# Kernel tuning notes

Hardware: AMD Instinct MI355X
Metric: run time of the kernel (lower is better)

The kernel has to match this reference:

```python
import jax, jax.numpy as jnp
import numpy as np

N = 100000      # nodes
E = 1600000     # edges (avg degree 16)
F_IN = 128      # num_features
H = 64          # hidden_dim
C = 7           # num_classes


def setup_inputs() -> dict:
    key = jax.random.key(0)
    ks = jax.random.split(key, 9)
    x = jax.random.normal(ks[0], (N, F_IN), dtype=jnp.float32)
    edge_index = jax.random.randint(ks[1], (2, E), 0, N, dtype=jnp.int32)
    s1 = 1.0 / np.sqrt(F_IN)
    s2 = 1.0 / np.sqrt(H)
    # SAGEConv1: lin_l applied to aggregated neighbors, lin_r to root
    W1l = jax.random.uniform(ks[2], (F_IN, H), jnp.float32, -s1, s1)
    W1r = jax.random.uniform(ks[3], (F_IN, H), jnp.float32, -s1, s1)
    b1 = jax.random.uniform(ks[4], (H,), jnp.float32, -s1, s1)
    # SAGEConv2
    W2l = jax.random.uniform(ks[5], (H, C), jnp.float32, -s2, s2)
    W2r = jax.random.uniform(ks[6], (H, C), jnp.float32, -s2, s2)
    b2 = jax.random.uniform(ks[7], (C,), jnp.float32, -s2, s2)
    return {"x": x, "edge_index": edge_index, "W1l": W1l, "W1r": W1r,
            "b1": b1, "W2l": W2l, "W2r": W2r, "b2": b2}


def _segment_mean(vals, idx, num_segments):
    # scatter-mean: sum messages per destination node, divide by in-degree
    sums = jax.ops.segment_sum(vals, idx, num_segments=num_segments)
    cnt = jax.ops.segment_sum(jnp.ones(idx.shape, vals.dtype), idx,
                              num_segments=num_segments)
    return sums / jnp.maximum(cnt, 1.0)[:, None]


def reference(x, edge_index, W1l, W1r, b1, W2l, W2r, b2):
    src, dst = edge_index[0], edge_index[1]
    # SAGEConv 1: mean of neighbor (src) features at each dst, plus root term
    agg1 = _segment_mean(x[src], dst, N)              # [N, F_IN]
    h = agg1 @ W1l + x @ W1r + b1                     # [N, H]
    h = jax.nn.relu(h)
    # dropout is inactive in eval mode (deterministic reference)
    # SAGEConv 2
    agg2 = _segment_mean(h[src], dst, N)              # [N, H]
    out = agg2 @ W2l + h @ W2r + b2                   # [N, C]
    return jax.nn.log_softmax(out, axis=1)
```

## Files before the change

### kernel.cpp

```cpp
#include <hip/hip_runtime.h>
#include <cstdint>
#include <cstddef>


#define CAP 64
#define BINSZ 128
#define CH 16384

typedef __attribute__((ext_vector_type(8))) short bf16x8v;
typedef __attribute__((ext_vector_type(4))) float f32x4v;

__device__ __forceinline__ float bf2f(unsigned short u) {
  return __uint_as_float(((unsigned int)u) << 16);
}
__device__ __forceinline__ unsigned short f2bf(float f) {
  unsigned int x = __float_as_uint(f);
  unsigned int r = (x + 0x7fffu + ((x >> 16) & 1u)) >> 16;
  return (unsigned short)r;
}

__global__ __launch_bounds__(256) void k_hist(const int* __restrict__ ei,
                                              int* __restrict__ hist,
                                              int E, int NB, int NCH) {
  __shared__ int lcnt[1024];
  const int c = blockIdx.x, t = threadIdx.x;
  for (int i = t; i < NB; i += 256) lcnt[i] = 0;
  __syncthreads();
  const int base = c * CH;
  const int end = min(base + CH, E);
  for (int e = base + t; e < end; e += 256) {
    int d = ei[E + e];
    atomicAdd(&lcnt[d >> 7], 1);
  }
  __syncthreads();
  for (int i = t; i < NB; i += 256) hist[(size_t)i * NCH + c] = lcnt[i];
}

__global__ __launch_bounds__(256) void k_scanA(int* __restrict__ hist,
                                               int* __restrict__ tot,
                                               int NB, int NCH) {
  const int lane = threadIdx.x & 63;
  const int bin = blockIdx.x * 4 + (threadIdx.x >> 6);
  if (bin >= NB) return;
  int* h = hist + (size_t)bin * NCH;
  int carry = 0;
  for (int base = 0; base < NCH; base += 64) {
    int i = base + lane;
    int v = (i < NCH) ? h[i] : 0;
    int incl = v;
    #pragma unroll
    for (int d = 1; d < 64; d <<= 1) {
      int t = __shfl_up(incl, d, 64);
      if (lane >= d) incl += t;
    }
    if (i < NCH) h[i] = carry + incl - v;
    carry += __shfl(incl, 63, 64);
  }
  if (lane == 0) tot[bin] = carry;
}

__global__ __launch_bounds__(64) void k_scanB(const int* __restrict__ tot,
                                              int* __restrict__ binbase, int NB) {
  const int lane = threadIdx.x;
  int carry = 0;
  for (int base = 0; base < NB; base += 64) {
    int i = base + lane;
    int v = (i < NB) ? tot[i] : 0;
    int incl = v;
    #pragma unroll
    for (int d = 1; d < 64; d <<= 1) {
      int t = __shfl_up(incl, d, 64);
      if (lane >= d) incl += t;
    }
    if (i < NB) binbase[i] = carry + incl - v;
    carry += __shfl(incl, 63, 64);
  }
  if (lane == 0) binbase[NB] = carry;
}

__global__ __launch_bounds__(256) void k_scat(const int* __restrict__ ei,
                                              const int* __restrict__ hist,
                                              const int* __restrict__ binbase,
                                              unsigned int* __restrict__ part,
                                              int E, int NB, int NCH) {
  __shared__ int lcur[1024];
  const int c = blockIdx.x, t = threadIdx.x;
  for (int i = t; i < NB; i += 256)
    lcur[i] = hist[(size_t)i * NCH + c] + binbase[i];
  __syncthreads();
  const int base = c * CH;
  const int end = min(base + CH, E);
  for (int e = base + t; e < end; e += 256) {
    int s = ei[e];
    int d = ei[E + e];
    int bin = d >> 7;
    int pos = atomicAdd(&lcur[bin], 1);
    part[pos] = (unsigned)s | ((unsigned)(d & 127) << 17);
  }
}

__global__ __launch_bounds__(256) void k_bucketB(const int* __restrict__ binbase,
                                                 const unsigned int* __restrict__ part,
                                                 int* __restrict__ cnt,
                                                 int* __restrict__ bucket) {
  __shared__ int lbkt[BINSZ * CAP];
  __shared__ int ldeg[BINSZ];
  const int b = blockIdx.x, t = threadIdx.x;
  if (t < BINSZ) ldeg[t] = 0;
  __syncthreads();
  const int e0 = binbase[b], e1 = binbase[b + 1];
  for (int i = e0 + t; i < e1; i += 256) {
    unsigned rec = part[i];
    int loc = rec >> 17;
    int p = atomicAdd(&ldeg[loc], 1);
    if (p < CAP) lbkt[loc * CAP + p] = (int)(rec & 0x1FFFFu);
  }
  __syncthreads();
  if (t < BINSZ) cnt[b * BINSZ + t] = ldeg[t];
  const int4* s4 = (const int4*)lbkt;
  int4* d4 = (int4*)(bucket + (size_t)b * BINSZ * CAP);
  #pragma unroll 2
  for (int i = t; i < BINSZ * CAP / 4; i += 256) d4[i] = s4[i];
}

__global__ __launch_bounds__(256) void k_wprep(const float* __restrict__ W1l,
                                               const float* __restrict__ W1r,
                                               unsigned short* __restrict__ wswz) {
  int idx = blockIdx.x * 256 + threadIdx.x;
  int j = idx & 7;
  int lane = (idx >> 3) & 63;
  int c = (idx >> 9) & 7;
  int t4 = idx >> 12;
  int kk = t4 * 32 + (lane >> 4) * 8 + j;
  int nn = c * 16 + (lane & 15);
  float v = (nn < 64) ? W1l[kk * 64 + nn] : W1r[kk * 64 + (nn - 64)];
  wswz[idx] = f2bf(v);
}

__global__ __launch_bounds__(256) void k_gemm1(
    const float* __restrict__ x,
    const unsigned short* __restrict__ wswz,
    const float* __restrict__ b1,
    unsigned short* __restrict__ xl,
    unsigned short* __restrict__ hroot,
    int Nn) {
  __shared__ unsigned short Bsw[16384];
  const int t = threadIdx.x;
  {
    const uint4* src = (const uint4*)wswz;
    uint4* dst = (uint4*)Bsw;
    #pragma unroll
    for (int i = 0; i < 8; ++i) dst[t + i * 256] = src[t + i * 256];
  }
  __syncthreads();

  const int lane = t & 63;
  const int wid = t >> 6;
  const int quad = lane >> 4;
  const int m = lane & 15;
  const int rowA = blockIdx.x * 64 + wid * 16 + m;
  const float* xrow = x + (size_t)min(rowA, Nn - 1) * 128;

  f32x4v acc[8];
  #pragma unroll
  for (int c = 0; c < 8; ++c) acc[c] = (f32x4v){0.f, 0.f, 0.f, 0.f};

  #pragma unroll
  for (int t4 = 0; t4 < 4; ++t4) {
    const int koff = t4 * 32 + quad * 8;
    float4 a0 = *(const float4*)(xrow + koff);
    float4 a1 = *(const float4*)(xrow + koff + 4);
    bf16x8v af;
    af[0] = (short)f2bf(a0.x); af[1] = (short)f2bf(a0.y);
    af[2] = (short)f2bf(a0.z); af[3] = (short)f2bf(a0.w);
    af[4] = (short)f2bf(a1.x); af[5] = (short)f2bf(a1.y);
    af[6] = (short)f2bf(a1.z); af[7] = (short)f2bf(a1.w);
    #pragma unroll
    for (int c = 0; c < 8; ++c) {
      const bf16x8v bf_ = *(const bf16x8v*)&Bsw[(((t4 * 8 + c) * 64 + lane)) << 3];
      acc[c] = __builtin_amdgcn_mfma_f32_16x16x32_bf16(af, bf_, acc[c], 0, 0, 0);
    }
  }

  const int rbase = blockIdx.x * 64 + wid * 16 + quad * 4;
  #pragma unroll
  for (int c = 0; c < 8; ++c) {
    const int col = c * 16 + m;
    #pragma unroll
    for (int i = 0; i < 4; ++i) {
      const int r = rbase + i;
      if (r < Nn) {
        if (c < 4) xl[(size_t)r * 64 + col] = f2bf(acc[c][i]);
        else       hroot[(size_t)r * 64 + (col - 64)] = f2bf(acc[c][i] + b1[col - 64]);
      }
    }
  }
}

__global__ __launch_bounds__(256) void k_agg1(
    const int* __restrict__ cnt, const int* __restrict__ bucket,
    const unsigned short* __restrict__ xl, const unsigned short* __restrict__ hroot,
    unsigned short* __restrict__ hbuf, int Nn) {
  const int lane = threadIdx.x & 63;
  const int gw = blockIdx.x * (blockDim.x >> 6) + (threadIdx.x >> 6);
  const int nw = gridDim.x * (blockDim.x >> 6);
  for (int n = gw; n < Nn; n += nw) {
    int c = cnt[n];
    int m = c < CAP ? c : CAP;
    int sidx = (lane < m) ? bucket[(size_t)n * CAP + lane] : 0;
    if ((unsigned)sidx >= (unsigned)Nn) sidx = 0;
    float acc = 0.f;
    int i = 0;
    for (; i + 4 <= m; i += 4) {
      int s0 = __shfl(sidx, i, 64);
      int s1 = __shfl(sidx, i + 1, 64);
      int s2 = __shfl(sidx, i + 2, 64);
      int s3 = __shfl(sidx, i + 3, 64);
      float v0 = bf2f(xl[(size_t)s0 * 64 + lane]);
      float v1 = bf2f(xl[(size_t)s1 * 64 + lane]);
      float v2 = bf2f(xl[(size_t)s2 * 64 + lane]);
      float v3 = bf2f(xl[(size_t)s3 * 64 + lane]);
      acc += (v0 + v1) + (v2 + v3);
    }
    for (; i < m; ++i) {
      int s = __shfl(sidx, i, 64);
      acc += bf2f(xl[(size_t)s * 64 + lane]);
    }
    float dd = c > 0 ? (float)c : 1.f;
    float hv = acc / dd + bf2f(hroot[(size_t)n * 64 + lane]);
    hbuf[(size_t)n * 64 + lane] = f2bf(fmaxf(hv, 0.f));
  }
}

__global__ __launch_bounds__(128) void k_gemm2(
    const unsigned short* __restrict__ hbuf,
    const float* __restrict__ W2l, const float* __restrict__ W2r,
    const float* __restrict__ b2,
    float* __restrict__ hl, float* __restrict__ hr, int Nn) {
  __shared__ float tile[128 * 65];
  const int t = threadIdx.x;
  const int rowbase = blockIdx.x * 128;
  for (int idx = t; idx < 128 * 64; idx += 128) {
    int r = idx >> 6, k = idx & 63;
    int n = rowbase + r;
    tile[r * 65 + k] = (n < Nn) ? bf2f(hbuf[(size_t)n * 64 + k]) : 0.f;
  }
  __syncthreads();
  int n = rowbase + t;
  if (n >= Nn) return;
  float al[7] = {0, 0, 0, 0, 0, 0, 0};
  float ar[7] = {0, 0, 0, 0, 0, 0, 0};
  for (int k = 0; k < 64; ++k) {
    float hv = tile[t * 65 + k];
    #pragma unroll
    for (int c = 0; c < 7; ++c) {
      al[c] = fmaf(hv, W2l[k * 7 + c], al[c]);
      ar[c] = fmaf(hv, W2r[k * 7 + c], ar[c]);
    }
  }
  #pragma unroll
  for (int c = 0; c < 7; ++c) {
    hl[(size_t)n * 7 + c] = al[c];
    hr[(size_t)n * 7 + c] = ar[c] + b2[c];
  }
}

__global__ __launch_bounds__(256) void k_out(
    const int* __restrict__ cnt, const int* __restrict__ bucket,
    const float* __restrict__ hl, const float* __restrict__ hr,
    float* __restrict__ out, int Nn) {
  const int lane = threadIdx.x & 63;
  const int c = lane & 7;
  const int sub = lane >> 3;
  const int gw = blockIdx.x * (blockDim.x >> 6) + (threadIdx.x >> 6);
  const int n = gw * 8 + sub;
  if (n >= Nn) return;
  int cn = cnt[n];
  int m = cn < CAP ? cn : CAP;
  const bool act = (c < 7);
  float acc = 0.f;
  for (int e = 0; e < m; ++e) {
    int s = bucket[(size_t)n * CAP + e];
    if ((unsigned)s >= (unsigned)Nn) s = 0;
    if (act) acc += hl[(size_t)s * 7 + c];
  }
  float dd = cn > 0 ? (float)cn : 1.f;
  float v = act ? (acc / dd + hr[(size_t)n * 7 + c]) : -INFINITY;
  float mx = v;
  mx = fmaxf(mx, __shfl_xor(mx, 1, 8));
  mx = fmaxf(mx, __shfl_xor(mx, 2, 8));
  mx = fmaxf(mx, __shfl_xor(mx, 4, 8));
  float ex = act ? expf(v - mx) : 0.f;
  float s2 = ex;
  s2 += __shfl_xor(s2, 1, 8);
  s2 += __shfl_xor(s2, 2, 8);
  s2 += __shfl_xor(s2, 4, 8);
  float res = v - mx - logf(s2);
  if (act) out[(size_t)n * 7 + c] = res;
}

static inline size_t alignup(size_t v) { return (v + 255) & ~(size_t)255; }

extern "C" void kernel_launch(void* const* d_in, const int* in_sizes, int n_in,
                              void* d_out, int out_size, void* d_ws, size_t ws_size,
                              hipStream_t stream) {
  const int N = in_sizes[0] / 128;
  const int E = in_sizes[1] / 2;
  const int NB = (N + BINSZ - 1) / BINSZ;
  const int Np = NB * BINSZ;
  const int NCH = (E + CH - 1) / CH;

  const float* x   = (const float*)d_in[0];
  const int*   ei  = (const int*)d_in[1];
  const float* W1l = (const float*)d_in[2];
  const float* W1r = (const float*)d_in[3];
  const float* b1  = (const float*)d_in[4];
  const float* W2l = (const float*)d_in[5];
  const float* W2r = (const float*)d_in[6];
  const float* b2  = (const float*)d_in[7];
  float* out = (float*)d_out;

  char* p = (char*)d_ws;
  int* hist    = (int*)p;            p += alignup((size_t)NB * NCH * 4);
  int* tot     = (int*)p;            p += alignup((size_t)NB * 4);
  int* binbase = (int*)p;            p += alignup((size_t)(NB + 1) * 4);
  unsigned int* part = (unsigned int*)p; p += alignup((size_t)E * 4);
  int* cnt    = (int*)p;             p += alignup((size_t)Np * 4);
  int* bucket = (int*)p;             p += alignup((size_t)Np * CAP * 4);
  unsigned short* wswz = (unsigned short*)p; p += alignup((size_t)16384 * 2);
  unsigned short* xl    = (unsigned short*)p; p += alignup((size_t)N * 64 * 2);
  unsigned short* hroot = (unsigned short*)p; p += alignup((size_t)N * 64 * 2);
  unsigned short* hbuf  = (unsigned short*)p; p += alignup((size_t)N * 64 * 2);
  float* hl  = (float*)p;            p += alignup((size_t)N * 7 * 4);
  float* hr  = (float*)p;            p += alignup((size_t)N * 7 * 4);

  dim3 b256(256);
  k_hist<<<dim3(NCH), b256, 0, stream>>>(ei, hist, E, NB, NCH);
  k_scanA<<<dim3((NB + 3) / 4), b256, 0, stream>>>(hist, tot, NB, NCH);
  k_scanB<<<dim3(1), dim3(64), 0, stream>>>(tot, binbase, NB);
  k_scat<<<dim3(NCH), b256, 0, stream>>>(ei, hist, binbase, part, E, NB, NCH);
  k_bucketB<<<dim3(NB), b256, 0, stream>>>(binbase, part, cnt, bucket);
  k_wprep<<<dim3(64), b256, 0, stream>>>(W1l, W1r, wswz);
  k_gemm1<<<dim3((N + 63) / 64), b256, 0, stream>>>(x, wswz, b1, xl, hroot, N);
  k_agg1<<<dim3(2048), b256, 0, stream>>>(cnt, bucket, xl, hroot, hbuf, N);
  k_gemm2<<<dim3((N + 127) / 128), dim3(128), 0, stream>>>(hbuf, W2l, W2r, b2, hl, hr, N);
  const int waves_out = (N + 7) / 8;
  k_out<<<dim3((waves_out + 3) / 4), b256, 0, stream>>>(cnt, bucket, hl, hr, out, N);
}
```

Baseline: 282.6 us.

## Aggregate directly from binned edge records with shared-memory atomics, drop bucket CSR

Removes the per-node bucket-building kernel and its capped 64-neighbor bucket array. Both aggregation stages now read the destination-binned edge records and accumulate into per-bin shared-memory float accumulators with LDS atomics. This avoids writing and re-reading a large padded bucket array and fixes the silent truncation at degree 64. In exchange it adds shared-atomic contention on high-degree nodes. It also pads hl/hr to 8 columns for aligned gathers and shrinks the histogram chunk size, which launches more histogram and scatter blocks.

```diff
diff --git a/kernel.cpp b/kernel.cpp
--- a/kernel.cpp
+++ b/kernel.cpp
@@ -3,9 +3,8 @@
 #include <cstddef>
 
 
-#define CAP 64
 #define BINSZ 128
-#define CH 16384
+#define CH 4096
 
 typedef __attribute__((ext_vector_type(8))) short bf16x8v;
 typedef __attribute__((ext_vector_type(4))) float f32x4v;
@@ -99,30 +98,6 @@
   }
 }
 
-__global__ __launch_bounds__(256) void k_bucketB(const int* __restrict__ binbase,
-                                                 const unsigned int* __restrict__ part,
-                                                 int* __restrict__ cnt,
-                                                 int* __restrict__ bucket) {
-  __shared__ int lbkt[BINSZ * CAP];
-  __shared__ int ldeg[BINSZ];
-  const int b = blockIdx.x, t = threadIdx.x;
-  if (t < BINSZ) ldeg[t] = 0;
-  __syncthreads();
-  const int e0 = binbase[b], e1 = binbase[b + 1];
-  for (int i = e0 + t; i < e1; i += 256) {
-    unsigned rec = part[i];
-    int loc = rec >> 17;
-    int p = atomicAdd(&ldeg[loc], 1);
-    if (p < CAP) lbkt[loc * CAP + p] = (int)(rec & 0x1FFFFu);
-  }
-  __syncthreads();
-  if (t < BINSZ) cnt[b * BINSZ + t] = ldeg[t];
-  const int4* s4 = (const int4*)lbkt;
-  int4* d4 = (int4*)(bucket + (size_t)b * BINSZ * CAP);
-  #pragma unroll 2
-  for (int i = t; i < BINSZ * CAP / 4; i += 256) d4[i] = s4[i];
-}
-
 __global__ __launch_bounds__(256) void k_wprep(const float* __restrict__ W1l,
                                                const float* __restrict__ W1r,
                                                unsigned short* __restrict__ wswz) {
@@ -197,38 +172,67 @@
   }
 }
 
-__global__ __launch_bounds__(256) void k_agg1(
-    const int* __restrict__ cnt, const int* __restrict__ bucket,
-    const unsigned short* __restrict__ xl, const unsigned short* __restrict__ hroot,
-    unsigned short* __restrict__ hbuf, int Nn) {
-  const int lane = threadIdx.x & 63;
-  const int gw = blockIdx.x * (blockDim.x >> 6) + (threadIdx.x >> 6);
-  const int nw = gridDim.x * (blockDim.x >> 6);
-  for (int n = gw; n < Nn; n += nw) {
-    int c = cnt[n];
-    int m = c < CAP ? c : CAP;
-    int sidx = (lane < m) ? bucket[(size_t)n * CAP + lane] : 0;
-    if ((unsigned)sidx >= (unsigned)Nn) sidx = 0;
-    float acc = 0.f;
-    int i = 0;
-    for (; i + 4 <= m; i += 4) {
-      int s0 = __shfl(sidx, i, 64);
-      int s1 = __shfl(sidx, i + 1, 64);
-      int s2 = __shfl(sidx, i + 2, 64);
-      int s3 = __shfl(sidx, i + 3, 64);
-      float v0 = bf2f(xl[(size_t)s0 * 64 + lane]);
-      float v1 = bf2f(xl[(size_t)s1 * 64 + lane]);
-      float v2 = bf2f(xl[(size_t)s2 * 64 + lane]);
-      float v3 = bf2f(xl[(size_t)s3 * 64 + lane]);
-      acc += (v0 + v1) + (v2 + v3);
-    }
-    for (; i < m; ++i) {
-      int s = __shfl(sidx, i, 64);
-      acc += bf2f(xl[(size_t)s * 64 + lane]);
-    }
-    float dd = c > 0 ? (float)c : 1.f;
-    float hv = acc / dd + bf2f(hroot[(size_t)n * 64 + lane]);
-    hbuf[(size_t)n * 64 + lane] = f2bf(fmaxf(hv, 0.f));
+__global__ __launch_bounds__(256) void k_aggF(
+    const int* __restrict__ binbase, const unsigned int* __restrict__ part,
+    const unsigned int* __restrict__ xl32, const unsigned int* __restrict__ hroot32,
+    unsigned int* __restrict__ hbuf32, int* __restrict__ cnt, int Nn) {
+  __shared__ float laccLo[BINSZ * 32];
+  __shared__ float laccHi[BINSZ * 32];
+  __shared__ int ldeg[BINSZ];
+  const int b = blockIdx.x, t = threadIdx.x;
+  for (int i = t; i < BINSZ * 32; i += 256) { laccLo[i] = 0.f; laccHi[i] = 0.f; }
+  if (t < BINSZ) ldeg[t] = 0;
+  __syncthreads();
+  const int e0 = binbase[b], e1 = binbase[b + 1];
+  const int p = t & 31;
+  int base = e0 + (t >> 5);
+  for (; base + 24 < e1; base += 32) {
+    unsigned rc0 = part[base];
+    unsigned rc1 = part[base + 8];
+    unsigned rc2 = part[base + 16];
+    unsigned rc3 = part[base + 24];
+    int s0 = rc0 & 0x1FFFF; if (s0 >= Nn) s0 = 0;
+    int s1 = rc1 & 0x1FFFF; if (s1 >= Nn) s1 = 0;
+    int s2 = rc2 & 0x1FFFF; if (s2 >= Nn) s2 = 0;
+    int s3 = rc3 & 0x1FFFF; if (s3 >= Nn) s3 = 0;
+    unsigned u0 = xl32[(size_t)s0 * 32 + p];
+    unsigned u1 = xl32[(size_t)s1 * 32 + p];
+    unsigned u2 = xl32[(size_t)s2 * 32 + p];
+    unsigned u3 = xl32[(size_t)s3 * 32 + p];
+    int l0 = rc0 >> 17, l1 = rc1 >> 17, l2 = rc2 >> 17, l3 = rc3 >> 17;
+    if (p == 0) {
+      atomicAdd(&ldeg[l0], 1); atomicAdd(&ldeg[l1], 1);
+      atomicAdd(&ldeg[l2], 1); atomicAdd(&ldeg[l3], 1);
+    }
+    unsafeAtomicAdd(&laccLo[l0 * 32 + p], __uint_as_float(u0 << 16));
+    unsafeAtomicAdd(&laccHi[l0 * 32 + p], __uint_as_float(u0 & 0xFFFF0000u));
+    unsafeAtomicAdd(&laccLo[l1 * 32 + p], __uint_as_float(u1 << 16));
+    unsafeAtomicAdd(&laccHi[l1 * 32 + p], __uint_as_float(u1 & 0xFFFF0000u));
+    unsafeAtomicAdd(&laccLo[l2 * 32 + p], __uint_as_float(u2 << 16));
+    unsafeAtomicAdd(&laccHi[l2 * 32 + p], __uint_as_float(u2 & 0xFFFF0000u));
+    unsafeAtomicAdd(&laccLo[l3 * 32 + p], __uint_as_float(u3 << 16));
+    unsafeAtomicAdd(&laccHi[l3 * 32 + p], __uint_as_float(u3 & 0xFFFF0000u));
+  }
+  for (; base < e1; base += 8) {
+    unsigned rc = part[base];
+    int s = rc & 0x1FFFF; if (s >= Nn) s = 0;
+    int loc = rc >> 17;
+    unsigned u = xl32[(size_t)s * 32 + p];
+    if (p == 0) atomicAdd(&ldeg[loc], 1);
+    unsafeAtomicAdd(&laccLo[loc * 32 + p], __uint_as_float(u << 16));
+    unsafeAtomicAdd(&laccHi[loc * 32 + p], __uint_as_float(u & 0xFFFF0000u));
+  }
+  __syncthreads();
+  if (t < BINSZ) cnt[b * BINSZ + t] = ldeg[t];
+  for (int r0 = (t >> 5); r0 < BINSZ; r0 += 8) {
+    int node = b * BINSZ + r0;
+    if (node >= Nn) continue;
+    int dg = ldeg[r0];
+    float dd = dg > 0 ? (float)dg : 1.f;
+    unsigned hu = hroot32[(size_t)node * 32 + p];
+    float h0 = fmaxf(laccLo[r0 * 32 + p] / dd + __uint_as_float(hu << 16), 0.f);
+    float h1 = fmaxf(laccHi[r0 * 32 + p] / dd + __uint_as_float(hu & 0xFFFF0000u), 0.f);
+    hbuf32[(size_t)node * 32 + p] = (unsigned)f2bf(h0) | ((unsigned)f2bf(h1) << 16);
   }
 }
 
@@ -260,43 +264,69 @@
   }
   #pragma unroll
   for (int c = 0; c < 7; ++c) {
-    hl[(size_t)n * 7 + c] = al[c];
-    hr[(size_t)n * 7 + c] = ar[c] + b2[c];
-  }
-}
-
-__global__ __launch_bounds__(256) void k_out(
-    const int* __restrict__ cnt, const int* __restrict__ bucket,
+    hl[(size_t)n * 8 + c] = al[c];
+    hr[(size_t)n * 8 + c] = ar[c] + b2[c];
+  }
+  hl[(size_t)n * 8 + 7] = 0.f;
+  hr[(size_t)n * 8 + 7] = 0.f;
+}
+
+__global__ __launch_bounds__(256) void k_outF(
+    const int* __restrict__ binbase, const unsigned int* __restrict__ part,
+    const int* __restrict__ cnt,
     const float* __restrict__ hl, const float* __restrict__ hr,
     float* __restrict__ out, int Nn) {
-  const int lane = threadIdx.x & 63;
-  const int c = lane & 7;
-  const int sub = lane >> 3;
-  const int gw = blockIdx.x * (blockDim.x >> 6) + (threadIdx.x >> 6);
-  const int n = gw * 8 + sub;
-  if (n >= Nn) return;
-  int cn = cnt[n];
-  int m = cn < CAP ? cn : CAP;
+  __shared__ float lout[BINSZ * 8];
+  const int b = blockIdx.x, t = threadIdx.x;
+  for (int i = t; i < BINSZ * 8; i += 256) lout[i] = 0.f;
+  __syncthreads();
+  const int e0 = binbase[b], e1 = binbase[b + 1];
+  const int c = t & 7;
+  int base = e0 + (t >> 3);
+  for (; base + 96 < e1; base += 128) {
+    unsigned rc0 = part[base];
+    unsigned rc1 = part[base + 32];
+    unsigned rc2 = part[base + 64];
+    unsigned rc3 = part[base + 96];
+    int s0 = rc0 & 0x1FFFF; if (s0 >= Nn) s0 = 0;
+    int s1 = rc1 & 0x1FFFF; if (s1 >= Nn) s1 = 0;
+    int s2 = rc2 & 0x1FFFF; if (s2 >= Nn) s2 = 0;
+    int s3 = rc3 & 0x1FFFF; if (s3 >= Nn) s3 = 0;
+    float v0 = hl[(size_t)s0 * 8 + c];
+    float v1 = hl[(size_t)s1 * 8 + c];
+    float v2 = hl[(size_t)s2 * 8 + c];
+    float v3 = hl[(size_t)s3 * 8 + c];
+    unsafeAtomicAdd(&lout[(rc0 >> 17) * 8 + c], v0);
+    unsafeAtomicAdd(&lout[(rc1 >> 17) * 8 + c], v1);
+    unsafeAtomicAdd(&lout[(rc2 >> 17) * 8 + c], v2);
+    unsafeAtomicAdd(&lout[(rc3 >> 17) * 8 + c], v3);
+  }
+  for (; base < e1; base += 32) {
+    unsigned rc = part[base];
+    int s = rc & 0x1FFFF; if (s >= Nn) s = 0;
+    unsafeAtomicAdd(&lout[(rc >> 17) * 8 + c], hl[(size_t)s * 8 + c]);
+  }
+  __syncthreads();
   const bool act = (c < 7);
-  float acc = 0.f;
-  for (int e = 0; e < m; ++e) {
-    int s = bucket[(size_t)n * CAP + e];
-    if ((unsigned)s >= (unsigned)Nn) s = 0;
-    if (act) acc += hl[(size_t)s * 7 + c];
-  }
-  float dd = cn > 0 ? (float)cn : 1.f;
-  float v = act ? (acc / dd + hr[(size_t)n * 7 + c]) : -INFINITY;
-  float mx = v;
-  mx = fmaxf(mx, __shfl_xor(mx, 1, 8));
-  mx = fmaxf(mx, __shfl_xor(mx, 2, 8));
-  mx = fmaxf(mx, __shfl_xor(mx, 4, 8));
-  float ex = act ? expf(v - mx) : 0.f;
-  float s2 = ex;
-  s2 += __shfl_xor(s2, 1, 8);
-  s2 += __shfl_xor(s2, 2, 8);
-  s2 += __shfl_xor(s2, 4, 8);
-  float res = v - mx - logf(s2);
-  if (act) out[(size_t)n * 7 + c] = res;
+  for (int r0 = (t >> 3); r0 < BINSZ; r0 += 32) {
+    int node = b * BINSZ + r0;
+    if (node >= Nn) continue;
+    int cn = cnt[b * BINSZ + r0];
+    float dd = cn > 0 ? (float)cn : 1.f;
+    float acc = lout[r0 * 8 + c];
+    float v = act ? (acc / dd + hr[(size_t)node * 8 + c]) : -INFINITY;
+    float mx = v;
+    mx = fmaxf(mx, __shfl_xor(mx, 1, 8));
+    mx = fmaxf(mx, __shfl_xor(mx, 2, 8));
+    mx = fmaxf(mx, __shfl_xor(mx, 4, 8));
+    float ex = act ? expf(v - mx) : 0.f;
+    float s2 = ex;
+    s2 += __shfl_xor(s2, 1, 8);
+    s2 += __shfl_xor(s2, 2, 8);
+    s2 += __shfl_xor(s2, 4, 8);
+    float res = v - mx - logf(s2);
+    if (act) out[(size_t)node * 7 + c] = res;
+  }
 }
 
 static inline size_t alignup(size_t v) { return (v + 255) & ~(size_t)255; }
@@ -326,24 +356,22 @@
   int* binbase = (int*)p;            p += alignup((size_t)(NB + 1) * 4);
   unsigned int* part = (unsigned int*)p; p += alignup((size_t)E * 4);
   int* cnt    = (int*)p;             p += alignup((size_t)Np * 4);
-  int* bucket = (int*)p;             p += alignup((size_t)Np * CAP * 4);
   unsigned short* wswz = (unsigned short*)p; p += alignup((size_t)16384 * 2);
   unsigned short* xl    = (unsigned short*)p; p += alignup((size_t)N * 64 * 2);
   unsigned short* hroot = (unsigned short*)p; p += alignup((size_t)N * 64 * 2);
   unsigned short* hbuf  = (unsigned short*)p; p += alignup((size_t)N * 64 * 2);
-  float* hl  = (float*)p;            p += alignup((size_t)N * 7 * 4);
-  float* hr  = (float*)p;            p += alignup((size_t)N * 7 * 4);
+  float* hl  = (float*)p;            p += alignup((size_t)N * 8 * 4);
+  float* hr  = (float*)p;            p += alignup((size_t)N * 8 * 4);
 
   dim3 b256(256);
   k_hist<<<dim3(NCH), b256, 0, stream>>>(ei, hist, E, NB, NCH);
   k_scanA<<<dim3((NB + 3) / 4), b256, 0, stream>>>(hist, tot, NB, NCH);
   k_scanB<<<dim3(1), dim3(64), 0, stream>>>(tot, binbase, NB);
   k_scat<<<dim3(NCH), b256, 0, stream>>>(ei, hist, binbase, part, E, NB, NCH);
-  k_bucketB<<<dim3(NB), b256, 0, stream>>>(binbase, part, cnt, bucket);
   k_wprep<<<dim3(64), b256, 0, stream>>>(W1l, W1r, wswz);
   k_gemm1<<<dim3((N + 63) / 64), b256, 0, stream>>>(x, wswz, b1, xl, hroot, N);
-  k_agg1<<<dim3(2048), b256, 0, stream>>>(cnt, bucket, xl, hroot, hbuf, N);
+  k_aggF<<<dim3(NB), b256, 0, stream>>>(binbase, part,
+      (const unsigned int*)xl, (const unsigned int*)hroot, (unsigned int*)hbuf, cnt, N);
   k_gemm2<<<dim3((N + 127) / 128), dim3(128), 0, stream>>>(hbuf, W2l, W2r, b2, hl, hr, N);
-  const int waves_out = (N + 7) / 8;
-  k_out<<<dim3((waves_out + 3) / 4), b256, 0, stream>>>(cnt, bucket, hl, hr, out, N);
-}
+  k_outF<<<dim3(NB), b256, 0, stream>>>(binbase, part, cnt, hl, hr, out, N);
+}
```

Measured after the change: 955.9 us. 238% more time.
